# Kernel tuning notes

Hardware: AMD Instinct MI355X
Metric: run time of the kernel (lower is better)

Reference implementation:

```python
import jax, jax.numpy as jnp
import numpy as np

N_RES = 768
DISTO_BINS = 64
LDDT_BINS = 50
MIN_RESOLUTION = 0.1
MAX_RESOLUTION = 3.0
W_DISTO, W_PLDDT, W_EXP = 0.3, 0.01, 0.01
CA_IDX = 1  # atom37 index of C-alpha


def setup_inputs() -> dict:
    key = jax.random.key(0)
    ks = jax.random.split(key, 6)
    B = 1
    return {
        "distogram_logits": jax.random.normal(ks[0], (B, N_RES, N_RES, DISTO_BINS), jnp.float32),
        "pseudo_beta": jax.random.normal(ks[1], (B, N_RES, 3), jnp.float32) * 10.0,
        "pseudo_beta_mask": jnp.ones((B, N_RES), jnp.float32),
        "lddt_logits": jax.random.normal(ks[2], (B, N_RES, LDDT_BINS), jnp.float32),
        "all_atom_pred_pos": jax.random.normal(ks[3], (B, N_RES, 37, 3), jnp.float32) * 10.0,
        "all_atom_positions": jax.random.normal(ks[4], (B, N_RES, 37, 3), jnp.float32) * 10.0,
        "all_atom_mask": jnp.ones((B, N_RES, 37), jnp.float32),
        "exp_resolved_logits": jax.random.normal(ks[5], (B, N_RES, 37), jnp.float32),
        "atom37_atom_exists": jnp.ones((B, N_RES, 37), jnp.float32),
        "resolution": jnp.ones((B,), jnp.float32),
    }


def _lddt(pred_pos, true_pos, mask, cutoff=15.0, eps=1e-10):
    # pred_pos/true_pos: [*, N, 3]; mask: [*, N, 1] -> per-residue lddt [*, N]
    n = mask.shape[-2]
    dmat_true = jnp.sqrt(eps + jnp.sum((true_pos[..., :, None, :] - true_pos[..., None, :, :]) ** 2, axis=-1))
    dmat_pred = jnp.sqrt(eps + jnp.sum((pred_pos[..., :, None, :] - pred_pos[..., None, :, :]) ** 2, axis=-1))
    scope = ((dmat_true < cutoff).astype(dmat_true.dtype)
             * mask * jnp.swapaxes(mask, -1, -2)
             * (1.0 - jnp.eye(n, dtype=dmat_true.dtype)))
    dist_l1 = jnp.abs(dmat_true - dmat_pred)
    score = 0.25 * ((dist_l1 < 0.5).astype(dist_l1.dtype) + (dist_l1 < 1.0)
                    + (dist_l1 < 2.0) + (dist_l1 < 4.0))
    norm = 1.0 / (eps + jnp.sum(scope, axis=-1))
    return norm * (eps + jnp.sum(scope * score, axis=-1))


def _ce_from_bins(logits, bins):
    # -sum(one_hot(bins) * log_softmax(logits)) == -log_softmax gathered at bins
    logp = jax.nn.log_softmax(logits, axis=-1)
    return -jnp.take_along_axis(logp, bins[..., None], axis=-1)[..., 0]


def _distogram_loss(logits, pseudo_beta, pseudo_beta_mask,
                    min_bin=2.3125, max_bin=21.6875, no_bins=DISTO_BINS, eps=1e-6):
    boundaries = jnp.linspace(min_bin, max_bin, no_bins - 1) ** 2
    d2 = jnp.sum((pseudo_beta[..., :, None, :] - pseudo_beta[..., None, :, :]) ** 2,
                 axis=-1, keepdims=True)  # [*, N, N, 1]
    true_bins = jnp.sum(d2 > boundaries, axis=-1).astype(jnp.int32)  # [*, N, N]
    errors = _ce_from_bins(logits, true_bins)
    sq_mask = pseudo_beta_mask[..., None] * pseudo_beta_mask[..., None, :]
    denom = eps + jnp.sum(sq_mask, axis=(-1, -2))
    mean = jnp.sum(errors * sq_mask, axis=-1) / denom[..., None]
    return jnp.mean(jnp.sum(mean, axis=-1))


def _lddt_loss(logits, all_atom_pred_pos, all_atom_positions, all_atom_mask, resolution,
               no_bins=LDDT_BINS, eps=1e-10):
    pred_ca = all_atom_pred_pos[..., CA_IDX, :]
    true_ca = all_atom_positions[..., CA_IDX, :]
    mask_ca = all_atom_mask[..., CA_IDX:CA_IDX + 1]  # [*, N, 1]
    score = jax.lax.stop_gradient(_lddt(pred_ca, true_ca, mask_ca, eps=eps))
    bin_idx = jnp.clip(jnp.floor(score * no_bins).astype(jnp.int32), 0, no_bins - 1)
    errors = _ce_from_bins(logits, bin_idx)
    m = mask_ca[..., 0]
    loss = jnp.sum(errors * m, axis=-1) / (eps + jnp.sum(m, axis=-1))
    gate = ((resolution >= MIN_RESOLUTION) & (resolution <= MAX_RESOLUTION)).astype(loss.dtype)
    return jnp.mean(loss * gate)


def _exp_resolved_loss(logits, atom37_atom_exists, all_atom_mask, resolution, eps=1e-8):
    errors = (-all_atom_mask * jax.nn.log_sigmoid(logits)
              - (1.0 - all_atom_mask) * jax.nn.log_sigmoid(-logits))
    loss = jnp.sum(errors * atom37_atom_exists, axis=-1)  # [*, N]
    loss = loss / (eps + jnp.sum(atom37_atom_exists, axis=(-1, -2)))[..., None]
    loss = jnp.sum(loss, axis=-1)
    gate = ((resolution >= MIN_RESOLUTION) & (resolution <= MAX_RESOLUTION)).astype(loss.dtype)
    return jnp.mean(loss * gate)


def reference(distogram_logits, pseudo_beta, pseudo_beta_mask, lddt_logits,
              all_atom_pred_pos, all_atom_positions, all_atom_mask,
              exp_resolved_logits, atom37_atom_exists, resolution):
    l_disto = _distogram_loss(distogram_logits, pseudo_beta, pseudo_beta_mask)
    l_plddt = _lddt_loss(lddt_logits, all_atom_pred_pos, all_atom_positions,
                         all_atom_mask, resolution)
    l_exp = _exp_resolved_loss(exp_resolved_logits, atom37_atom_exists,
                               all_atom_mask, resolution)
    return W_DISTO * l_disto + W_PLDDT * l_plddt + W_EXP * l_exp
```

## Files before the change

### kernel.cpp

```cpp
#include <hip/hip_runtime.h>
#include <math.h>

#define N_RES 768
#define DISTO_BINS 64
#define LDDT_BINS 50
#define DISTO_GRID 2048
#define EXP_GRID 64

__global__ __launch_bounds__(256)
void disto_partial_kernel(const float4* __restrict__ logits4,
                          const float* __restrict__ pb,
                          const float* __restrict__ pbm,
                          float* __restrict__ partial) {
    __shared__ float spb[N_RES * 3];
    __shared__ float spm[N_RES];
    for (int k = threadIdx.x; k < N_RES * 3; k += blockDim.x) spb[k] = pb[k];
    for (int k = threadIdx.x; k < N_RES; k += blockDim.x) spm[k] = pbm[k];
    __syncthreads();

    const int lane = threadIdx.x & 63;
    const int wid  = threadIdx.x >> 6;
    const int q    = lane >> 4;
    const int gl   = lane & 15;
    const int gw   = blockIdx.x * 4 + wid;
    const int nw   = DISTO_GRID * 4;
    const int nchunks = (N_RES * N_RES) / 4;

    float acc = 0.f;

#define DISTO_PROC(xv4, cc)                                                   \
    {                                                                         \
        float e = __expf(xv4.x) + __expf(xv4.y) + __expf(xv4.z) +             \
                  __expf(xv4.w);                                              \
        e += __shfl_xor(e, 1, 64);                                            \
        e += __shfl_xor(e, 2, 64);                                            \
        e += __shfl_xor(e, 4, 64);                                            \
        e += __shfl_xor(e, 8, 64);                                            \
        int p = (cc) * 4 + q;                                                 \
        int i = p / N_RES;                                                    \
        int j = p - i * N_RES;                                                \
        float dx = spb[3 * i + 0] - spb[3 * j + 0];                           \
        float dy = spb[3 * i + 1] - spb[3 * j + 1];                           \
        float dz = spb[3 * i + 2] - spb[3 * j + 2];                           \
        float d  = sqrtf(dx * dx + dy * dy + dz * dz);                        \
        float t  = ceilf((d - 2.3125f) * 3.2f);                               \
        int bin  = (int)fminf(fmaxf(t, 0.f), 63.f);                           \
        float xs = (bin & 2) ? ((bin & 1) ? xv4.w : xv4.z)                    \
                             : ((bin & 1) ? xv4.y : xv4.x);                   \
        float xv = __shfl(xs, (q << 4) + (bin >> 2), 64);                     \
        if (gl == 0) acc += (__logf(e) - xv) * spm[i] * spm[j];               \
    }

    for (int c0 = gw; c0 < nchunks; c0 += 4 * nw) {
        const int c1 = c0 + nw;
        const int c2 = c0 + 2 * nw;
        const int c3 = c0 + 3 * nw;
        float4 x0 = logits4[(size_t)c0 * 64 + lane];
        float4 x1 = (c1 < nchunks) ? logits4[(size_t)c1 * 64 + lane]
                                   : make_float4(0.f, 0.f, 0.f, 0.f);
        float4 x2 = (c2 < nchunks) ? logits4[(size_t)c2 * 64 + lane]
                                   : make_float4(0.f, 0.f, 0.f, 0.f);
        float4 x3 = (c3 < nchunks) ? logits4[(size_t)c3 * 64 + lane]
                                   : make_float4(0.f, 0.f, 0.f, 0.f);

        DISTO_PROC(x0, c0);
        if (c1 < nchunks) DISTO_PROC(x1, c1);
        if (c2 < nchunks) DISTO_PROC(x2, c2);
        if (c3 < nchunks) DISTO_PROC(x3, c3);
    }
#undef DISTO_PROC

    acc += __shfl_xor(acc, 16, 64);
    acc += __shfl_xor(acc, 32, 64);
    __shared__ float wsum[4];
    if (lane == 0) wsum[wid] = acc;
    __syncthreads();
    if (threadIdx.x == 0)
        partial[blockIdx.x] = wsum[0] + wsum[1] + wsum[2] + wsum[3];
}

__global__ __launch_bounds__(128)
void small_losses_kernel(const float* __restrict__ pred37,
                         const float* __restrict__ true37,
                         const float* __restrict__ mask37,
                         const float* __restrict__ lddt_logits,
                         const float* __restrict__ exl,
                         const float* __restrict__ a37ex,
                         float* __restrict__ errm,
                         float* __restrict__ expnum,
                         float* __restrict__ expden) {
    const int tid  = threadIdx.x;
    const int nthr = blockDim.x;
    __shared__ float r1[128], r2[128];

    if (blockIdx.x >= N_RES) {
        const int b = blockIdx.x - N_RES;
        const int gid = b * nthr + tid;
        const int stride = EXP_GRID * nthr;
        const int n = N_RES * 37;
        float num = 0.f, den = 0.f;
        for (int k = gid; k < n; k += stride) {
            float x  = exl[k];
            float m  = mask37[k];
            float ex = a37ex[k];
            float ax = fabsf(x);
            float sp = __logf(1.f + __expf(-ax));
            float ls  = sp + fmaxf(-x, 0.f);
            float lsn = sp + fmaxf(x, 0.f);
            float err = m * ls + (1.f - m) * lsn;
            num += err * ex;
            den += ex;
        }
        r1[tid] = num;
        r2[tid] = den;
        __syncthreads();
        for (int s = nthr >> 1; s > 0; s >>= 1) {
            if (tid < s) { r1[tid] += r1[tid + s]; r2[tid] += r2[tid + s]; }
            __syncthreads();
        }
        if (tid == 0) { expnum[b] = r1[0]; expden[b] = r2[0]; }
        return;
    }

    const int i = blockIdx.x;
    const float tix = true37[(i * 37 + 1) * 3 + 0];
    const float tiy = true37[(i * 37 + 1) * 3 + 1];
    const float tiz = true37[(i * 37 + 1) * 3 + 2];
    const float pix = pred37[(i * 37 + 1) * 3 + 0];
    const float piy = pred37[(i * 37 + 1) * 3 + 1];
    const float piz = pred37[(i * 37 + 1) * 3 + 2];
    const float mi  = mask37[i * 37 + 1];

    float scope_sum = 0.f, score_sum = 0.f;
    for (int j = tid; j < N_RES; j += nthr) {
        float mj  = mask37[j * 37 + 1];
        float dtx = tix - true37[(j * 37 + 1) * 3 + 0];
        float dty = tiy - true37[(j * 37 + 1) * 3 + 1];
        float dtz = tiz - true37[(j * 37 + 1) * 3 + 2];
        float dt  = sqrtf(1e-10f + dtx * dtx + dty * dty + dtz * dtz);
        float dpx = pix - pred37[(j * 37 + 1) * 3 + 0];
        float dpy = piy - pred37[(j * 37 + 1) * 3 + 1];
        float dpz = piz - pred37[(j * 37 + 1) * 3 + 2];
        float dp  = sqrtf(1e-10f + dpx * dpx + dpy * dpy + dpz * dpz);
        float scope = (dt < 15.f && j != i) ? (mi * mj) : 0.f;
        float l1 = fabsf(dt - dp);
        float sc = 0.25f * ((l1 < 0.5f ? 1.f : 0.f) + (l1 < 1.f ? 1.f : 0.f) +
                            (l1 < 2.f ? 1.f : 0.f) + (l1 < 4.f ? 1.f : 0.f));
        scope_sum += scope;
        score_sum += scope * sc;
    }

    r1[tid] = scope_sum;
    r2[tid] = score_sum;
    __syncthreads();
    for (int s = nthr >> 1; s > 0; s >>= 1) {
        if (tid < s) { r1[tid] += r1[tid + s]; r2[tid] += r2[tid + s]; }
        __syncthreads();
    }

    __shared__ int binS;
    if (tid == 0) {
        float lddt = (1e-10f + r2[0]) / (1e-10f + r1[0]);
        int bin = (int)floorf(lddt * (float)LDDT_BINS);
        binS = min(max(bin, 0), LDDT_BINS - 1);
    }
    __syncthreads();

    float e = (tid < LDDT_BINS) ? __expf(lddt_logits[i * LDDT_BINS + tid]) : 0.f;
    r1[tid] = e;
    __syncthreads();
    for (int s = nthr >> 1; s > 0; s >>= 1) {
        if (tid < s) r1[tid] += r1[tid + s];
        __syncthreads();
    }
    if (tid == 0) {
        float err = __logf(r1[0]) - lddt_logits[i * LDDT_BINS + binS];
        errm[i] = err * mi;
    }
}

__global__ __launch_bounds__(256)
void finalize_kernel(const float* __restrict__ partial,
                     const float* __restrict__ pbm,
                     const float* __restrict__ errm,
                     const float* __restrict__ mask37,
                     const float* __restrict__ expnum,
                     const float* __restrict__ expden,
                     const float* __restrict__ resolution,
                     float* __restrict__ out) {
    const int tid = threadIdx.x;
    const int nthr = blockDim.x;

    double sd = 0.0, sm = 0.0, se = 0.0, smca = 0.0, num = 0.0, den = 0.0;
    for (int k = tid; k < DISTO_GRID; k += nthr) sd += (double)partial[k];
    for (int k = tid; k < N_RES; k += nthr) {
        sm   += (double)pbm[k];
        se   += (double)errm[k];
        smca += (double)mask37[k * 37 + 1];
    }
    if (tid < EXP_GRID) { num = (double)expnum[tid]; den = (double)expden[tid]; }

    __shared__ double red[256];
    double vals[6] = {sd, sm, se, smca, num, den};
    double tot[6];
    for (int v = 0; v < 6; ++v) {
        red[tid] = vals[v];
        __syncthreads();
        for (int s = nthr >> 1; s > 0; s >>= 1) {
            if (tid < s) red[tid] += red[tid + s];
            __syncthreads();
        }
        tot[v] = red[0];
        __syncthreads();
    }

    if (tid == 0) {
        float res = resolution[0];
        double gate = (res >= 0.1f && res <= 3.0f) ? 1.0 : 0.0;
        double l_disto = tot[0] / (1e-6 + tot[1] * tot[1]);
        double l_plddt = tot[2] / (1e-10 + tot[3]) * gate;
        double l_exp   = tot[4] / (1e-8 + tot[5]) * gate;
        out[0] = (float)(0.3 * l_disto + 0.01 * l_plddt + 0.01 * l_exp);
    }
}

extern "C" void kernel_launch(void* const* d_in, const int* in_sizes, int n_in,
                              void* d_out, int out_size, void* d_ws, size_t ws_size,
                              hipStream_t stream) {
    const float* disto       = (const float*)d_in[0];
    const float* pb          = (const float*)d_in[1];
    const float* pbm         = (const float*)d_in[2];
    const float* lddt_logits = (const float*)d_in[3];
    const float* pred        = (const float*)d_in[4];
    const float* truep       = (const float*)d_in[5];
    const float* am          = (const float*)d_in[6];
    const float* exl         = (const float*)d_in[7];
    const float* a37         = (const float*)d_in[8];
    const float* resolution  = (const float*)d_in[9];
    float* out = (float*)d_out;

    float* ws      = (float*)d_ws;
    float* partial = ws;
    float* errm    = ws + DISTO_GRID;
    float* expnum  = errm + N_RES;
    float* expden  = expnum + EXP_GRID;

    disto_partial_kernel<<<DISTO_GRID, 256, 0, stream>>>(
        (const float4*)disto, pb, pbm, partial);
    small_losses_kernel<<<N_RES + EXP_GRID, 128, 0, stream>>>(
        pred, truep, am, lddt_logits, exl, a37, errm, expnum, expden);
    finalize_kernel<<<1, 256, 0, stream>>>(partial, pbm, errm, am,
                                           expnum, expden, resolution, out);
}
```

Baseline: 253.9 us.

## Precompute pair bins and weights in separate kernel; use DPP row reductions

Adds a pre-pass kernel that computes each residue pair's distance bin (as a byte) and mask weight (as a float) into workspace. The main distogram kernel then loads these instead of recomputing distances from shared memory. It also replaces the xor-shuffle row sums with DPP row-rotate adds and swaps the gather-shuffle of the target logit for per-lane predicated accumulation, with one full wave reduction at the end. The aim is to cut ALU and LDS work in the bandwidth-bound main loop, at the cost of an extra launch and roughly 3 MB of extra memory traffic for bins and weights.

```diff
diff --git a/kernel.cpp b/kernel.cpp
--- a/kernel.cpp
+++ b/kernel.cpp
@@ -6,25 +6,43 @@
 #define LDDT_BINS 50
 #define DISTO_GRID 2048
 #define EXP_GRID 64
+#define NPAIRS (N_RES * N_RES)
+#define NCHUNKS (NPAIRS / 4)
+
+#define ROW_ADD_ROR(v, N)                                                     \
+    v += __int_as_float(__builtin_amdgcn_update_dpp(                          \
+        0, __float_as_int(v), 0x120 | (N), 0xF, 0xF, false))
+
+__global__ __launch_bounds__(256)
+void pair_meta_kernel(const float* __restrict__ pb,
+                      const float* __restrict__ pbm,
+                      unsigned char* __restrict__ bins,
+                      float* __restrict__ wgt) {
+    int p = blockIdx.x * blockDim.x + threadIdx.x;
+    if (p >= NPAIRS) return;
+    int i = p / N_RES;
+    int j = p - i * N_RES;
+    float dx = pb[3 * i + 0] - pb[3 * j + 0];
+    float dy = pb[3 * i + 1] - pb[3 * j + 1];
+    float dz = pb[3 * i + 2] - pb[3 * j + 2];
+    float d  = sqrtf(dx * dx + dy * dy + dz * dz);
+    float t  = ceilf((d - 2.3125f) * 3.2f);
+    int bin  = (int)fminf(fmaxf(t, 0.f), 63.f);
+    bins[p]  = (unsigned char)bin;
+    wgt[p]   = pbm[i] * pbm[j];
+}
 
 __global__ __launch_bounds__(256)
 void disto_partial_kernel(const float4* __restrict__ logits4,
-                          const float* __restrict__ pb,
-                          const float* __restrict__ pbm,
+                          const unsigned int* __restrict__ binw,
+                          const float* __restrict__ wgt,
                           float* __restrict__ partial) {
-    __shared__ float spb[N_RES * 3];
-    __shared__ float spm[N_RES];
-    for (int k = threadIdx.x; k < N_RES * 3; k += blockDim.x) spb[k] = pb[k];
-    for (int k = threadIdx.x; k < N_RES; k += blockDim.x) spm[k] = pbm[k];
-    __syncthreads();
-
     const int lane = threadIdx.x & 63;
     const int wid  = threadIdx.x >> 6;
     const int q    = lane >> 4;
     const int gl   = lane & 15;
     const int gw   = blockIdx.x * 4 + wid;
     const int nw   = DISTO_GRID * 4;
-    const int nchunks = (N_RES * N_RES) / 4;
 
     float acc = 0.f;
 
@@ -32,44 +50,43 @@
     {                                                                         \
         float e = __expf(xv4.x) + __expf(xv4.y) + __expf(xv4.z) +             \
                   __expf(xv4.w);                                              \
-        e += __shfl_xor(e, 1, 64);                                            \
-        e += __shfl_xor(e, 2, 64);                                            \
-        e += __shfl_xor(e, 4, 64);                                            \
-        e += __shfl_xor(e, 8, 64);                                            \
-        int p = (cc) * 4 + q;                                                 \
-        int i = p / N_RES;                                                    \
-        int j = p - i * N_RES;                                                \
-        float dx = spb[3 * i + 0] - spb[3 * j + 0];                           \
-        float dy = spb[3 * i + 1] - spb[3 * j + 1];                           \
-        float dz = spb[3 * i + 2] - spb[3 * j + 2];                           \
-        float d  = sqrtf(dx * dx + dy * dy + dz * dz);                        \
-        float t  = ceilf((d - 2.3125f) * 3.2f);                               \
-        int bin  = (int)fminf(fmaxf(t, 0.f), 63.f);                           \
+        ROW_ADD_ROR(e, 8);                                                    \
+        ROW_ADD_ROR(e, 4);                                                    \
+        ROW_ADD_ROR(e, 2);                                                    \
+        ROW_ADD_ROR(e, 1);                                                    \
+        unsigned int bw = binw[cc];                                           \
+        int bin = (int)((bw >> (q * 8)) & 63u);                               \
+        float w  = wgt[(cc) * 4 + q];                                         \
         float xs = (bin & 2) ? ((bin & 1) ? xv4.w : xv4.z)                    \
                              : ((bin & 1) ? xv4.y : xv4.x);                   \
-        float xv = __shfl(xs, (q << 4) + (bin >> 2), 64);                     \
-        if (gl == 0) acc += (__logf(e) - xv) * spm[i] * spm[j];               \
-    }
-
-    for (int c0 = gw; c0 < nchunks; c0 += 4 * nw) {
+        float lg = (gl == 0) ? w * __logf(e) : 0.f;                           \
+        float bt = (gl == (bin >> 2)) ? w * xs : 0.f;                         \
+        acc += lg - bt;                                                       \
+    }
+
+    for (int c0 = gw; c0 < NCHUNKS; c0 += 4 * nw) {
         const int c1 = c0 + nw;
         const int c2 = c0 + 2 * nw;
         const int c3 = c0 + 3 * nw;
         float4 x0 = logits4[(size_t)c0 * 64 + lane];
-        float4 x1 = (c1 < nchunks) ? logits4[(size_t)c1 * 64 + lane]
+        float4 x1 = (c1 < NCHUNKS) ? logits4[(size_t)c1 * 64 + lane]
                                    : make_float4(0.f, 0.f, 0.f, 0.f);
-        float4 x2 = (c2 < nchunks) ? logits4[(size_t)c2 * 64 + lane]
+        float4 x2 = (c2 < NCHUNKS) ? logits4[(size_t)c2 * 64 + lane]
                                    : make_float4(0.f, 0.f, 0.f, 0.f);
-        float4 x3 = (c3 < nchunks) ? logits4[(size_t)c3 * 64 + lane]
+        float4 x3 = (c3 < NCHUNKS) ? logits4[(size_t)c3 * 64 + lane]
                                    : make_float4(0.f, 0.f, 0.f, 0.f);
 
         DISTO_PROC(x0, c0);
-        if (c1 < nchunks) DISTO_PROC(x1, c1);
-        if (c2 < nchunks) DISTO_PROC(x2, c2);
-        if (c3 < nchunks) DISTO_PROC(x3, c3);
+        if (c1 < NCHUNKS) DISTO_PROC(x1, c1);
+        if (c2 < NCHUNKS) DISTO_PROC(x2, c2);
+        if (c3 < NCHUNKS) DISTO_PROC(x3, c3);
     }
 #undef DISTO_PROC
 
+    acc += __shfl_xor(acc, 1, 64);
+    acc += __shfl_xor(acc, 2, 64);
+    acc += __shfl_xor(acc, 4, 64);
+    acc += __shfl_xor(acc, 8, 64);
     acc += __shfl_xor(acc, 16, 64);
     acc += __shfl_xor(acc, 32, 64);
     __shared__ float wsum[4];
@@ -244,9 +261,12 @@
     float* errm    = ws + DISTO_GRID;
     float* expnum  = errm + N_RES;
     float* expden  = expnum + EXP_GRID;
-
+    float* wgt     = ws + 4096;
+    unsigned char* bins = (unsigned char*)(wgt + NPAIRS);
+
+    pair_meta_kernel<<<(NPAIRS + 255) / 256, 256, 0, stream>>>(pb, pbm, bins, wgt);
     disto_partial_kernel<<<DISTO_GRID, 256, 0, stream>>>(
-        (const float4*)disto, pb, pbm, partial);
+        (const float4*)disto, (const unsigned int*)bins, wgt, partial);
     small_losses_kernel<<<N_RES + EXP_GRID, 128, 0, stream>>>(
         pred, truep, am, lddt_logits, exl, a37, errm, expnum, expden);
     finalize_kernel<<<1, 256, 0, stream>>>(partial, pbm, errm, am,
```

New measurement: 251.6 us. No clear change (-0.9%).
